# Kernel optimization log

Measured on AMD Instinct MI355X. Metric: run time of the kernel, lower is better.

The kernel has to match this reference:

```python
import jax, jax.numpy as jnp
import numpy as np

N_NODES = 100000
N_EDGES = 640000
D = 128
N_LAYERS = 4
N_GRAPHS = 512


def setup_inputs() -> dict:
    key = jax.random.key(0)
    ks = jax.random.split(key, 12)
    x = jax.random.normal(ks[0], (N_NODES, D), dtype=jnp.float32)
    edge_index = jax.random.randint(ks[1], (2, N_EDGES), 0, N_NODES, dtype=jnp.int64)
    batch = jnp.sort(jax.random.randint(ks[2], (N_NODES,), 0, N_GRAPHS, dtype=jnp.int64))
    s = 1.0 / np.sqrt(D)
    convW = jax.random.uniform(ks[3], (N_LAYERS, D, D), jnp.float32, -s, s)
    convB = jax.random.uniform(ks[4], (N_LAYERS, D), jnp.float32, -s, s)
    W1 = jax.random.uniform(ks[5], (D, D), jnp.float32, -s, s)
    b1 = jax.random.uniform(ks[6], (D,), jnp.float32, -s, s)
    W2 = jax.random.uniform(ks[7], (D, D), jnp.float32, -s, s)
    b2 = jax.random.uniform(ks[8], (D,), jnp.float32, -s, s)
    W3 = jax.random.uniform(ks[9], (D, 1), jnp.float32, -s, s)
    b3 = jax.random.uniform(ks[10], (1,), jnp.float32, -s, s)
    return {"x": x, "edge_index": edge_index, "batch": batch,
            "convW": convW, "convB": convB,
            "W1": W1, "b1": b1, "W2": W2, "b2": b2, "W3": W3, "b3": b3}


def reference(x, edge_index, batch, convW, convB, W1, b1, W2, b2, W3, b3):
    N = x.shape[0]
    # GCNConv default: add self-loops, symmetric deg^-1/2 normalization
    loops = jnp.arange(N, dtype=edge_index.dtype)
    src = jnp.concatenate([edge_index[0], loops])  # [E+N]
    dst = jnp.concatenate([edge_index[1], loops])
    deg = jax.ops.segment_sum(jnp.ones_like(dst, dtype=x.dtype), dst, num_segments=N)
    dinv = jnp.where(deg > 0, jax.lax.rsqrt(deg), 0.0)
    norm = (dinv[src] * dinv[dst])[:, None]  # [E+N, 1]
    h = x
    for i in range(N_LAYERS):
        hw = h @ convW[i]                                   # [N, D]
        msg = hw[src] * norm                                # gather + scale [E+N, D]
        agg = jax.ops.segment_sum(msg, dst, num_segments=N)  # scatter-add [N, D]
        h = jax.nn.relu(agg + convB[i])
    pooled = jax.ops.segment_sum(h, batch, num_segments=N_GRAPHS)  # [G, D]
    z = jax.nn.relu(pooled @ W1 + b1)
    z = jax.nn.relu(z @ W2 + b2)
    return jax.nn.sigmoid(z @ W3 + b3)  # [G, 1]
```

## Files before the change

### kernel.cpp

```cpp
#include <hip/hip_runtime.h>
#include <math.h>

#define D 128
#define LSTRIDE 136

typedef _Float16 half8 __attribute__((ext_vector_type(8)));
typedef _Float16 half4v __attribute__((ext_vector_type(4)));
typedef float f32x4 __attribute__((ext_vector_type(4)));


__global__ void k_fat1(const int* __restrict__ ei, int* __restrict__ counts,
                       int* __restrict__ pidx, int E, int countBlocks,
                       const float* __restrict__ convW, _Float16* __restrict__ Wf) {
    if ((int)blockIdx.x < countBlocks) {
        int e0 = (blockIdx.x * blockDim.x + threadIdx.x) * 4;
        if (e0 + 3 < E) {
            int4 d4 = *(const int4*)(ei + E + e0);
            int4 p;
            p.x = atomicAdd(&counts[d4.x], 1);
            p.y = atomicAdd(&counts[d4.y], 1);
            p.z = atomicAdd(&counts[d4.z], 1);
            p.w = atomicAdd(&counts[d4.w], 1);
            *(int4*)(pidx + e0) = p;
        } else {
            for (int e = e0; e < E; e++) pidx[e] = atomicAdd(&counts[ei[E + e]], 1);
        }
    } else {
        const int bid = blockIdx.x - countBlocks;
        const int l = bid >> 3;
        const int slot = (bid & 7) * 256 + threadIdx.x;
        const float* W = convW + (size_t)l * D * D;
        const int p = slot >> 6, ln = slot & 63;
        const int s = p >> 3, c = p & 7;
        const int kbase = s * 32 + ((ln >> 4) << 3);
        const int n = (c << 4) + (ln & 15);
        half8 hv;
#pragma unroll
        for (int j = 0; j < 8; j++) hv[j] = (_Float16)W[(size_t)(kbase + j) * D + n];
        *(half8*)(Wf + (size_t)l * D * D + (size_t)slot * 8) = hv;
    }
}

__global__ __launch_bounds__(256) void k_scan1(const int* __restrict__ counts,
                                               int* __restrict__ rowptrP,
                                               int* __restrict__ bsums,
                                               float* __restrict__ dinv,
                                               int* __restrict__ degHist, int N) {
    __shared__ int sh[256];
    __shared__ int lh[64];
    const int t = threadIdx.x;
    const int base = blockIdx.x * 1024 + t * 4;
    int c[4], pj[4];
#pragma unroll
    for (int j = 0; j < 4; j++) {
        c[j] = (base + j < N) ? counts[base + j] : 0;
        pj[j] = (c[j] + 3) & ~3;
    }
#pragma unroll
    for (int j = 0; j < 4; j++)
        if (base + j < N) dinv[base + j] = rsqrtf((float)(c[j] + 1));

    if (t < 64) lh[t] = 0;
    __syncthreads();
#pragma unroll
    for (int j = 0; j < 4; j++)
        if (base + j < N) atomicAdd(&lh[c[j] < 63 ? c[j] : 63], 1);
    __syncthreads();
    if (t < 64 && lh[t]) atomicAdd(&degHist[t], lh[t]);

    int tsum = pj[0] + pj[1] + pj[2] + pj[3];
    sh[t] = tsum;
    __syncthreads();
    for (int off = 1; off < 256; off <<= 1) {
        int v = (t >= off) ? sh[t - off] : 0;
        __syncthreads();
        sh[t] += v;
        __syncthreads();
    }
    int run = (t == 0) ? 0 : sh[t - 1];
    if (t == 255) bsums[blockIdx.x] = sh[255];
#pragma unroll
    for (int j = 0; j < 4; j++) {
        if (base + j <= N) rowptrP[base + j] = run;
        run += pj[j];
    }
}


__global__ __launch_bounds__(256) void k_fat2(int* __restrict__ rowptrP,
                                              const int* __restrict__ counts,
                                              const int* __restrict__ bsums,
                                              int NB, int N, int scanBlocks, int NS,
                                              int* __restrict__ srcs,
                                              const int* __restrict__ degHist,
                                              int* __restrict__ degCur,
                                              int* __restrict__ perm,
                                              int* __restrict__ rankOf) {
    if ((int)blockIdx.x < scanBlocks) {
        __shared__ int pre[128];
        const int t = threadIdx.x;
        if (t < 128) pre[t] = (t < NB) ? bsums[t] : 0;
        __syncthreads();
        for (int off = 1; off < 128; off <<= 1) {
            int v = (t >= off && t < 128) ? pre[t - off] : 0;
            __syncthreads();
            if (t < 128) pre[t] += v;
            __syncthreads();
        }
        int i = blockIdx.x * blockDim.x + t;
        if (i <= N) {
            int b = i >> 10;
            int add = (b == 0) ? 0 : pre[b - 1];
            int rp = rowptrP[i] + add;
            rowptrP[i] = rp;
            if (i < N) {
                int c = counts[i];
                int re_ = rp + c;
                int pad = (-c) & 3;
                for (int k2 = 0; k2 < pad; k2++) srcs[re_ + k2] = NS;
            }
        }
    } else {
        __shared__ int lbase[64], lh[64], gb[64];
        const int t = threadIdx.x;
        const int i = ((int)blockIdx.x - scanBlocks) * blockDim.x + t;
        if (t < 64) lh[t] = 0;
        __syncthreads();
        int deg = 0, lrank = 0;
        const bool v = i < N;
        if (v) {
            int c = counts[i];
            deg = c < 63 ? c : 63;
            lrank = atomicAdd(&lh[deg], 1);
        }
        __syncthreads();
        if (t < 64) gb[t] = lh[t] ? atomicAdd(&degCur[t], lh[t]) : 0;
        if (t == 0) {
            int run = 0;
            for (int d = 63; d >= 0; d--) { lbase[d] = run; run += degHist[d]; }
        }
        __syncthreads();
        if (v) {
            int r = lbase[deg] + gb[deg] + lrank;
            perm[r] = i;
            rankOf[i] = r;
        }
    }
}


__global__ void k_fill(const int* __restrict__ ei, const int* __restrict__ rowptrP,
                       const int* __restrict__ pidx, int* __restrict__ srcs, int E,
                       int fillBlocks, int slotBlocks, int N, int NS,
                       const int* __restrict__ rankOf,
                       const int* __restrict__ perm,
                       const float* __restrict__ dinv,
                       int* __restrict__ rbegR, int* __restrict__ rpenR,
                       float* __restrict__ dinvR, int* __restrict__ sentIdx,
                       const float* __restrict__ x,
                       _Float16* __restrict__ gA, _Float16* __restrict__ gB) {
    const int b = blockIdx.x;
    if (b < fillBlocks) {
        int e0 = (b * blockDim.x + threadIdx.x) * 4;
        if (e0 + 3 < E) {
            int4 s4 = *(const int4*)(ei + e0);
            int4 d4 = *(const int4*)(ei + E + e0);
            int4 p4 = *(const int4*)(pidx + e0);
            srcs[rowptrP[d4.x] + p4.x] = rankOf[s4.x];
            srcs[rowptrP[d4.y] + p4.y] = rankOf[s4.y];
            srcs[rowptrP[d4.z] + p4.z] = rankOf[s4.z];
            srcs[rowptrP[d4.w] + p4.w] = rankOf[s4.w];
        } else {
            for (int e = e0; e < E; e++)
                srcs[rowptrP[ei[E + e]] + pidx[e]] = rankOf[ei[e]];
        }
    } else if (b < fillBlocks + slotBlocks) {
        const int r = (b - fillBlocks) * blockDim.x + threadIdx.x;
        if (r == 0) { int4 sv; sv.x = sv.y = sv.z = sv.w = NS; *(int4*)sentIdx = sv; }
        if (r < NS) {
            if (r < N) {
                int p = perm[r];
                rbegR[r] = rowptrP[p];
                rpenR[r] = rowptrP[p + 1];
                dinvR[r] = dinv[p];
            } else {
                rbegR[r] = 0; rpenR[r] = 0; dinvR[r] = 0.f;
            }
        }
    } else {
        const int i = (b - fillBlocks - slotBlocks) * blockDim.x + threadIdx.x;
        const int TC = (NS + 1) * 16;
        if (i >= TC) return;
        const int row = i >> 4, j = i & 15;
        if (row < N) {
            const float s = dinv[row];
            const int rr = rankOf[row];
            const float4 v0 = *(const float4*)(x + (size_t)row * D + j * 8);
            const float4 v1 = *(const float4*)(x + (size_t)row * D + j * 8 + 4);
            half8 h;
            h[0] = (_Float16)(v0.x * s); h[1] = (_Float16)(v0.y * s);
            h[2] = (_Float16)(v0.z * s); h[3] = (_Float16)(v0.w * s);
            h[4] = (_Float16)(v1.x * s); h[5] = (_Float16)(v1.y * s);
            h[6] = (_Float16)(v1.z * s); h[7] = (_Float16)(v1.w * s);
            *(half8*)(gA + (size_t)rr * D + j * 8) = h;
        } else {
            half8 z;
#pragma unroll
            for (int j2 = 0; j2 < 8; j2++) z[j2] = (_Float16)0.f;
            *(half8*)(gA + (size_t)row * D + j * 8) = z;
            *(half8*)(gB + (size_t)row * D + j * 8) = z;
        }
    }
}


__global__ __launch_bounds__(256) void k_layer(
        const _Float16* __restrict__ gin,
        const int* __restrict__ rbegR, const int* __restrict__ rpenR,
        const int* __restrict__ srcs,
        const int* __restrict__ sentIdx,
        const float* __restrict__ dinvR,
        const int* __restrict__ perm,
        const _Float16* __restrict__ Wf,
        const float* __restrict__ bias,
        _Float16* __restrict__ gout, int N, int last) {
    __shared__ _Float16 S[64 * LSTRIDE];
    __shared__ _Float16 WL[D * D];

    const int tid  = threadIdx.x;
    const int w    = tid >> 6;
    const int lane = tid & 63;
    const int q    = lane >> 4;
    const int l16  = lane & 15;
    const int sb   = blockIdx.x * 64;
    const int cb   = l16 * 8;
    const int slot0 = sb + w * 16 + q * 4;

#pragma unroll 2
    for (int i = 0; i < 8; i++) {
        const int slot = i * 256 + tid;
        half8 wv = *(const half8*)(Wf + (size_t)slot * 8);
        *(half8*)(&WL[(size_t)slot * 8]) = wv;
    }

    int bg[4], nc[4];
    int mx = 0;
#pragma unroll
    for (int it = 0; it < 4; it++) {
        bg[it] = rbegR[slot0 + it];
        nc[it] = (rpenR[slot0 + it] - bg[it]) >> 2;
        mx = nc[it] > mx ? nc[it] : mx;
    }

    float a[4][8];
#pragma unroll
    for (int it = 0; it < 4; it++) {
        half8 sv = *(const half8*)(gin + (size_t)(slot0 + it) * D + cb);
#pragma unroll
        for (int j = 0; j < 8; j++) a[it][j] = (float)sv[j];
    }

    int4 cur[4];
#pragma unroll
    for (int it = 0; it < 4; it++) {
        const int* ip = (0 < nc[it]) ? (srcs + bg[it]) : sentIdx;
        cur[it] = *(const int4*)ip;
    }
    for (int ch = 0; ch < mx; ch++) {
        int4 nxt[4];
#pragma unroll
        for (int it = 0; it < 4; it++) {
            const int* ip = (ch + 1 < nc[it]) ? (srcs + bg[it] + (ch + 1) * 4) : sentIdx;
            nxt[it] = *(const int4*)ip;
        }
#pragma unroll
        for (int it = 0; it < 4; it++) {
            half8 v0 = *(const half8*)(gin + (size_t)cur[it].x * D + cb);
            half8 v1 = *(const half8*)(gin + (size_t)cur[it].y * D + cb);
            half8 v2 = *(const half8*)(gin + (size_t)cur[it].z * D + cb);
            half8 v3 = *(const half8*)(gin + (size_t)cur[it].w * D + cb);
#pragma unroll
            for (int j = 0; j < 8; j++)
                a[it][j] += ((float)v0[j] + (float)v1[j]) + ((float)v2[j] + (float)v3[j]);
        }
#pragma unroll
        for (int it = 0; it < 4; it++) cur[it] = nxt[it];
    }

#pragma unroll
    for (int it = 0; it < 4; it++) {
        const float sc = dinvR[slot0 + it];
        const int nl = w * 16 + q * 4 + it;
        half8 o;
#pragma unroll
        for (int j = 0; j < 8; j++) o[j] = (_Float16)(a[it][j] * sc);
        *(half8*)(&S[nl * LSTRIDE + cb]) = o;
    }

    __syncthreads();

    f32x4 acc[8];
#pragma unroll
    for (int cc = 0; cc < 8; cc++) acc[cc] = (f32x4){0.f, 0.f, 0.f, 0.f};

    const int nl2 = w * 16 + l16;
#pragma unroll
    for (int s = 0; s < 4; s++) {
        half8 bf = *(const half8*)(&S[nl2 * LSTRIDE + s * 32 + q * 8]);
#pragma unroll
        for (int cc = 0; cc < 8; cc++) {
            half8 wh = *(const half8*)(&WL[(size_t)((s * 8 + cc) * 64 + lane) * 8]);
            acc[cc] = __builtin_amdgcn_mfma_f32_16x16x32_f16(wh, bf, acc[cc], 0, 0, 0);
        }
    }

    const int slot2 = sb + nl2;
    if (!last) {
        const float scale = dinvR[slot2];
        _Float16* rp = gout + (size_t)slot2 * D + q * 4;
#pragma unroll
        for (int cc = 0; cc < 8; cc++) {
            const float4 bc = *(const float4*)(bias + cc * 16 + q * 4);
            half4v o;
            o[0] = (_Float16)(fmaxf(acc[cc][0] + bc.x, 0.f) * scale);
            o[1] = (_Float16)(fmaxf(acc[cc][1] + bc.y, 0.f) * scale);
            o[2] = (_Float16)(fmaxf(acc[cc][2] + bc.z, 0.f) * scale);
            o[3] = (_Float16)(fmaxf(acc[cc][3] + bc.w, 0.f) * scale);
            *(half4v*)(rp + cc * 16) = o;
        }
    } else if (slot2 < N) {
        const int node2 = perm[slot2];
        _Float16* rp = gout + (size_t)node2 * D + q * 4;
#pragma unroll
        for (int cc = 0; cc < 8; cc++) {
            const float4 bc = *(const float4*)(bias + cc * 16 + q * 4);
            half4v o;
            o[0] = (_Float16)fmaxf(acc[cc][0] + bc.x, 0.f);
            o[1] = (_Float16)fmaxf(acc[cc][1] + bc.y, 0.f);
            o[2] = (_Float16)fmaxf(acc[cc][2] + bc.z, 0.f);
            o[3] = (_Float16)fmaxf(acc[cc][3] + bc.w, 0.f);
            *(half4v*)(rp + cc * 16) = o;
        }
    }
}


__global__ __launch_bounds__(256) void k_poolhead(
        const _Float16* __restrict__ h, const int* __restrict__ batch,
        const float* __restrict__ W1, const float* __restrict__ b1,
        const float* __restrict__ W2, const float* __restrict__ b2,
        const float* __restrict__ W3, const float* __restrict__ b3,
        float* __restrict__ out, int N) {
    __shared__ int sb[2];
    __shared__ float part[16][D];
    __shared__ float pool[D];
    __shared__ float z[D];
    __shared__ float red[D];
    __shared__ float pr[2][D];

    const int g = blockIdx.x;
    const int t = threadIdx.x;

    if (t < 2) {
        int target = g + t;
        int lo = 0, hi = N;
        while (lo < hi) {
            int mid = (lo + hi) >> 1;
            if (batch[mid] < target) lo = mid + 1; else hi = mid;
        }
        sb[t] = lo;
    }
    __syncthreads();
    const int rs = sb[0], re = sb[1];

    const int w = t >> 6;
    const int lane = t & 63;
    const int rw = w * 4 + (lane >> 4);
    const int c8 = (lane & 15) * 8;

    float ax[8];
#pragma unroll
    for (int j = 0; j < 8; j++) ax[j] = 0.f;
    for (int r = rs + rw; r < re; r += 16) {
        half8 vv = *(const half8*)(h + (size_t)r * D + c8);
#pragma unroll
        for (int j = 0; j < 8; j++) ax[j] += (float)vv[j];
    }
#pragma unroll
    for (int j = 0; j < 8; j++) part[rw][c8 + j] = ax[j];
    __syncthreads();

    if (t < D) {
        float s = 0.f;
#pragma unroll
        for (int gg = 0; gg < 16; gg++) s += part[gg][t];
        pool[t] = s;
    }
    __syncthreads();

    {
        const int hf = t >> 7, tt = t & 127;
        const int k0 = hf * 64;
        float s = 0.f;
        for (int k = k0; k < k0 + 64; k++) s = fmaf(pool[k], W1[(size_t)k * D + tt], s);
        pr[hf][tt] = s;
    }
    __syncthreads();
    if (t < D) z[t] = fmaxf(pr[0][t] + pr[1][t] + b1[t], 0.f);
    __syncthreads();

    {
        const int hf = t >> 7, tt = t & 127;
        const int k0 = hf * 64;
        float s = 0.f;
        for (int k = k0; k < k0 + 64; k++) s = fmaf(z[k], W2[(size_t)k * D + tt], s);
        pr[hf][tt] = s;
    }
    __syncthreads();
    if (t < D) red[t] = fmaxf(pr[0][t] + pr[1][t] + b2[t], 0.f) * W3[t];
    __syncthreads();
    for (int off = 64; off >= 1; off >>= 1) {
        if (t < off) red[t] += red[t + off];
        __syncthreads();
    }
    if (t == 0) out[g] = 1.f / (1.f + expf(-(red[0] + b3[0])));
}


extern "C" void kernel_launch(void* const* d_in, const int* in_sizes, int n_in,
                              void* d_out, int out_size, void* d_ws, size_t ws_size,
                              hipStream_t stream) {
    const float* x     = (const float*)d_in[0];
    const int*   ei    = (const int*)d_in[1];
    const int*   batch = (const int*)d_in[2];
    const float* convW = (const float*)d_in[3];
    const float* convB = (const float*)d_in[4];
    const float* W1 = (const float*)d_in[5];
    const float* b1 = (const float*)d_in[6];
    const float* W2 = (const float*)d_in[7];
    const float* b2 = (const float*)d_in[8];
    const float* W3 = (const float*)d_in[9];
    const float* b3 = (const float*)d_in[10];
    float* out = (float*)d_out;

    const int N = in_sizes[0] / D;
    const int E = in_sizes[1] / 2;
    const int G = out_size;
    const int NB = (N + 1023) / 1024;
    const int NS = ((N + 63) / 64) * 64;

    char* w = (char*)d_ws;
    size_t off = 0;
    auto alloc = [&](size_t bytes) -> char* {
        char* p = w + off;
        off += (bytes + 255) & ~(size_t)255;
        return p;
    };
    float*     dinv   = (float*)alloc((size_t)N * 4);
    _Float16*  gA     = (_Float16*)alloc((size_t)(NS + 1) * D * 2);
    _Float16*  gB     = (_Float16*)alloc((size_t)(NS + 1) * D * 2);
    _Float16*  Wf     = (_Float16*)alloc((size_t)4 * D * D * 2);
    int*       counts = (int*)alloc((size_t)(N + 128) * 4);
    int*       degHist= counts + N;
    int*       degCur = counts + N + 64;
    int*       rowptrP= (int*)alloc((size_t)(N + 1) * 4);
    int*       pidx   = (int*)alloc((size_t)E * 4);
    int*       srcs   = (int*)alloc((size_t)(E + 3 * N) * 4);
    int*       bsums  = (int*)alloc((size_t)NB * 4);
    int*       perm   = (int*)alloc((size_t)N * 4);
    int*       rankOf = (int*)alloc((size_t)N * 4);
    int*       rbegR  = (int*)alloc((size_t)NS * 4);
    int*       rpenR  = (int*)alloc((size_t)NS * 4);
    float*     dinvR  = (float*)alloc((size_t)NS * 4);
    int*       sentIdx= (int*)alloc(16);

    hipMemsetAsync(counts, 0, (size_t)(N + 128) * 4, stream);
    const int countBlocks = (E / 4 + 255) / 256;
    k_fat1<<<countBlocks + 32, 256, 0, stream>>>(ei, counts, pidx, E, countBlocks,
                                                 convW, Wf);
    k_scan1<<<NB, 256, 0, stream>>>(counts, rowptrP, bsums, dinv, degHist, N);
    const int scanBlocks = (N + 1 + 255) / 256;
    const int rankBlocks = (N + 255) / 256;
    k_fat2<<<scanBlocks + rankBlocks, 256, 0, stream>>>(rowptrP, counts, bsums, NB, N,
                                                        scanBlocks, NS, srcs,
                                                        degHist, degCur, perm, rankOf);
    const int fillBlocks = (E / 4 + 255) / 256;
    const int slotBlocks = (NS + 255) / 256;
    const int cvtBlocks  = ((NS + 1) * 16 + 255) / 256;
    k_fill<<<fillBlocks + slotBlocks + cvtBlocks, 256, 0, stream>>>(
        ei, rowptrP, pidx, srcs, E, fillBlocks, slotBlocks, N, NS,
        rankOf, perm, dinv, rbegR, rpenR, dinvR, sentIdx, x, gA, gB);

    const int layer_grid = NS / 64;
    const _Float16* gi = gA;
    _Float16* go = gB;
    for (int l = 0; l < 4; l++) {
        k_layer<<<layer_grid, 256, 0, stream>>>(gi, rbegR, rpenR, srcs, sentIdx,
                                                dinvR, perm,
                                                Wf + (size_t)l * D * D,
                                                convB + (size_t)l * D,
                                                go, N, l == 3);
        const _Float16* tmp = go;
        go = (_Float16*)gi;
        gi = tmp;
    }

    k_poolhead<<<G, 256, 0, stream>>>(gi, batch, W1, b1, W2, b2, W3, b3, out, N);
}
```

Before: 358.7 us.

## Halve layer tile size, read weights from global, merge fill row work

```diff
diff --git a/kernel.cpp b/kernel.cpp
--- a/kernel.cpp
+++ b/kernel.cpp
@@ -151,7 +151,7 @@
 
 __global__ void k_fill(const int* __restrict__ ei, const int* __restrict__ rowptrP,
                        const int* __restrict__ pidx, int* __restrict__ srcs, int E,
-                       int fillBlocks, int slotBlocks, int N, int NS,
+                       int fillBlocks, int N, int NS,
                        const int* __restrict__ rankOf,
                        const int* __restrict__ perm,
                        const float* __restrict__ dinv,
@@ -174,29 +174,37 @@
             for (int e = e0; e < E; e++)
                 srcs[rowptrP[ei[E + e]] + pidx[e]] = rankOf[ei[e]];
         }
-    } else if (b < fillBlocks + slotBlocks) {
-        const int r = (b - fillBlocks) * blockDim.x + threadIdx.x;
-        if (r == 0) { int4 sv; sv.x = sv.y = sv.z = sv.w = NS; *(int4*)sentIdx = sv; }
-        if (r < NS) {
+    } else {
+        __shared__ int pS[16];
+        __shared__ float dS[16];
+        const int base = (b - fillBlocks) * 16;
+        const int t = threadIdx.x;
+        if (t == 0 && base == 0) {
+            int4 sv; sv.x = sv.y = sv.z = sv.w = NS; *(int4*)sentIdx = sv;
+        }
+        if (t < 16) {
+            const int r = base + t;
+            int p = -1; float dv = 0.f;
             if (r < N) {
-                int p = perm[r];
+                p = perm[r];
                 rbegR[r] = rowptrP[p];
                 rpenR[r] = rowptrP[p + 1];
-                dinvR[r] = dinv[p];
-            } else {
+                dv = dinv[p];
+                dinvR[r] = dv;
+            } else if (r < NS) {
                 rbegR[r] = 0; rpenR[r] = 0; dinvR[r] = 0.f;
             }
-        }
-    } else {
-        const int i = (b - fillBlocks - slotBlocks) * blockDim.x + threadIdx.x;
-        const int TC = (NS + 1) * 16;
-        if (i >= TC) return;
-        const int row = i >> 4, j = i & 15;
-        if (row < N) {
-            const float s = dinv[row];
-            const int rr = rankOf[row];
-            const float4 v0 = *(const float4*)(x + (size_t)row * D + j * 8);
-            const float4 v1 = *(const float4*)(x + (size_t)row * D + j * 8 + 4);
+            pS[t] = p; dS[t] = dv;
+        }
+        __syncthreads();
+        const int rr = base + (t >> 4);
+        if (rr > NS) return;
+        const int j = t & 15;
+        const int p = pS[t >> 4];
+        if (p >= 0) {
+            const float s = dS[t >> 4];
+            const float4 v0 = *(const float4*)(x + (size_t)p * D + j * 8);
+            const float4 v1 = *(const float4*)(x + (size_t)p * D + j * 8 + 4);
             half8 h;
             h[0] = (_Float16)(v0.x * s); h[1] = (_Float16)(v0.y * s);
             h[2] = (_Float16)(v0.z * s); h[3] = (_Float16)(v0.w * s);
@@ -207,14 +215,14 @@
             half8 z;
 #pragma unroll
             for (int j2 = 0; j2 < 8; j2++) z[j2] = (_Float16)0.f;
-            *(half8*)(gA + (size_t)row * D + j * 8) = z;
-            *(half8*)(gB + (size_t)row * D + j * 8) = z;
-        }
-    }
-}
-
-
-__global__ __launch_bounds__(256) void k_layer(
+            *(half8*)(gA + (size_t)rr * D + j * 8) = z;
+            *(half8*)(gB + (size_t)rr * D + j * 8) = z;
+        }
+    }
+}
+
+
+__global__ __launch_bounds__(256, 8) void k_layer(
         const _Float16* __restrict__ gin,
         const int* __restrict__ rbegR, const int* __restrict__ rpenR,
         const int* __restrict__ srcs,
@@ -224,57 +232,49 @@
         const _Float16* __restrict__ Wf,
         const float* __restrict__ bias,
         _Float16* __restrict__ gout, int N, int last) {
-    __shared__ _Float16 S[64 * LSTRIDE];
-    __shared__ _Float16 WL[D * D];
+    __shared__ _Float16 S[32 * LSTRIDE];
 
     const int tid  = threadIdx.x;
     const int w    = tid >> 6;
     const int lane = tid & 63;
     const int q    = lane >> 4;
     const int l16  = lane & 15;
-    const int sb   = blockIdx.x * 64;
+    const int sb   = blockIdx.x * 32;
     const int cb   = l16 * 8;
-    const int slot0 = sb + w * 16 + q * 4;
-
-#pragma unroll 2
-    for (int i = 0; i < 8; i++) {
-        const int slot = i * 256 + tid;
-        half8 wv = *(const half8*)(Wf + (size_t)slot * 8);
-        *(half8*)(&WL[(size_t)slot * 8]) = wv;
-    }
-
-    int bg[4], nc[4];
+    const int slot0 = sb + w * 8 + q * 2;
+
+    int bg[2], nc[2];
     int mx = 0;
 #pragma unroll
-    for (int it = 0; it < 4; it++) {
+    for (int it = 0; it < 2; it++) {
         bg[it] = rbegR[slot0 + it];
         nc[it] = (rpenR[slot0 + it] - bg[it]) >> 2;
         mx = nc[it] > mx ? nc[it] : mx;
     }
 
-    float a[4][8];
-#pragma unroll
-    for (int it = 0; it < 4; it++) {
+    float a[2][8];
+#pragma unroll
+    for (int it = 0; it < 2; it++) {
         half8 sv = *(const half8*)(gin + (size_t)(slot0 + it) * D + cb);
 #pragma unroll
         for (int j = 0; j < 8; j++) a[it][j] = (float)sv[j];
     }
 
-    int4 cur[4];
-#pragma unroll
-    for (int it = 0; it < 4; it++) {
+    int4 cur[2];
+#pragma unroll
+    for (int it = 0; it < 2; it++) {
         const int* ip = (0 < nc[it]) ? (srcs + bg[it]) : sentIdx;
         cur[it] = *(const int4*)ip;
     }
     for (int ch = 0; ch < mx; ch++) {
-        int4 nxt[4];
-#pragma unroll
-        for (int it = 0; it < 4; it++) {
+        int4 nxt[2];
+#pragma unroll
+        for (int it = 0; it < 2; it++) {
             const int* ip = (ch + 1 < nc[it]) ? (srcs + bg[it] + (ch + 1) * 4) : sentIdx;
             nxt[it] = *(const int4*)ip;
         }
 #pragma unroll
-        for (int it = 0; it < 4; it++) {
+        for (int it = 0; it < 2; it++) {
             half8 v0 = *(const half8*)(gin + (size_t)cur[it].x * D + cb);
             half8 v1 = *(const half8*)(gin + (size_t)cur[it].y * D + cb);
             half8 v2 = *(const half8*)(gin + (size_t)cur[it].z * D + cb);
@@ -284,13 +284,13 @@
                 a[it][j] += ((float)v0[j] + (float)v1[j]) + ((float)v2[j] + (float)v3[j]);
         }
 #pragma unroll
-        for (int it = 0; it < 4; it++) cur[it] = nxt[it];
-    }
-
-#pragma unroll
-    for (int it = 0; it < 4; it++) {
+        for (int it = 0; it < 2; it++) cur[it] = nxt[it];
+    }
+
+#pragma unroll
+    for (int it = 0; it < 2; it++) {
         const float sc = dinvR[slot0 + it];
-        const int nl = w * 16 + q * 4 + it;
+        const int nl = w * 8 + q * 2 + it;
         half8 o;
 #pragma unroll
         for (int j = 0; j < 8; j++) o[j] = (_Float16)(a[it][j] * sc);
@@ -299,18 +299,20 @@
 
     __syncthreads();
 
-    f32x4 acc[8];
-#pragma unroll
-    for (int cc = 0; cc < 8; cc++) acc[cc] = (f32x4){0.f, 0.f, 0.f, 0.f};
-
-    const int nl2 = w * 16 + l16;
+    f32x4 acc[4];
+#pragma unroll
+    for (int c2 = 0; c2 < 4; c2++) acc[c2] = (f32x4){0.f, 0.f, 0.f, 0.f};
+
+    const int tile = w >> 1;
+    const int ccb  = (w & 1) * 4;
+    const int nl2  = tile * 16 + l16;
 #pragma unroll
     for (int s = 0; s < 4; s++) {
         half8 bf = *(const half8*)(&S[nl2 * LSTRIDE + s * 32 + q * 8]);
 #pragma unroll
-        for (int cc = 0; cc < 8; cc++) {
-            half8 wh = *(const half8*)(&WL[(size_t)((s * 8 + cc) * 64 + lane) * 8]);
-            acc[cc] = __builtin_amdgcn_mfma_f32_16x16x32_f16(wh, bf, acc[cc], 0, 0, 0);
+        for (int c2 = 0; c2 < 4; c2++) {
+            half8 wh = *(const half8*)(Wf + (size_t)((s * 8 + ccb + c2) * 64 + lane) * 8);
+            acc[c2] = __builtin_amdgcn_mfma_f32_16x16x32_f16(wh, bf, acc[c2], 0, 0, 0);
         }
     }
 
@@ -319,26 +321,28 @@
         const float scale = dinvR[slot2];
         _Float16* rp = gout + (size_t)slot2 * D + q * 4;
 #pragma unroll
-        for (int cc = 0; cc < 8; cc++) {
+        for (int c2 = 0; c2 < 4; c2++) {
+            const int cc = ccb + c2;
             const float4 bc = *(const float4*)(bias + cc * 16 + q * 4);
             half4v o;
-            o[0] = (_Float16)(fmaxf(acc[cc][0] + bc.x, 0.f) * scale);
-            o[1] = (_Float16)(fmaxf(acc[cc][1] + bc.y, 0.f) * scale);
-            o[2] = (_Float16)(fmaxf(acc[cc][2] + bc.z, 0.f) * scale);
-            o[3] = (_Float16)(fmaxf(acc[cc][3] + bc.w, 0.f) * scale);
+            o[0] = (_Float16)(fmaxf(acc[c2][0] + bc.x, 0.f) * scale);
+            o[1] = (_Float16)(fmaxf(acc[c2][1] + bc.y, 0.f) * scale);
+            o[2] = (_Float16)(fmaxf(acc[c2][2] + bc.z, 0.f) * scale);
+            o[3] = (_Float16)(fmaxf(acc[c2][3] + bc.w, 0.f) * scale);
             *(half4v*)(rp + cc * 16) = o;
         }
     } else if (slot2 < N) {
         const int node2 = perm[slot2];
         _Float16* rp = gout + (size_t)node2 * D + q * 4;
 #pragma unroll
-        for (int cc = 0; cc < 8; cc++) {
+        for (int c2 = 0; c2 < 4; c2++) {
+            const int cc = ccb + c2;
             const float4 bc = *(const float4*)(bias + cc * 16 + q * 4);
             half4v o;
-            o[0] = (_Float16)fmaxf(acc[cc][0] + bc.x, 0.f);
-            o[1] = (_Float16)fmaxf(acc[cc][1] + bc.y, 0.f);
-            o[2] = (_Float16)fmaxf(acc[cc][2] + bc.z, 0.f);
-            o[3] = (_Float16)fmaxf(acc[cc][3] + bc.w, 0.f);
+            o[0] = (_Float16)fmaxf(acc[c2][0] + bc.x, 0.f);
+            o[1] = (_Float16)fmaxf(acc[c2][1] + bc.y, 0.f);
+            o[2] = (_Float16)fmaxf(acc[c2][2] + bc.z, 0.f);
+            o[3] = (_Float16)fmaxf(acc[c2][3] + bc.w, 0.f);
             *(half4v*)(rp + cc * 16) = o;
         }
     }
@@ -485,13 +489,12 @@
                                                         scanBlocks, NS, srcs,
                                                         degHist, degCur, perm, rankOf);
     const int fillBlocks = (E / 4 + 255) / 256;
-    const int slotBlocks = (NS + 255) / 256;
-    const int cvtBlocks  = ((NS + 1) * 16 + 255) / 256;
-    k_fill<<<fillBlocks + slotBlocks + cvtBlocks, 256, 0, stream>>>(
-        ei, rowptrP, pidx, srcs, E, fillBlocks, slotBlocks, N, NS,
+    const int rowBlocks  = (NS + 16) / 16;
+    k_fill<<<fillBlocks + rowBlocks, 256, 0, stream>>>(
+        ei, rowptrP, pidx, srcs, E, fillBlocks, N, NS,
         rankOf, perm, dinv, rbegR, rpenR, dinvR, sentIdx, x, gA, gB);
 
-    const int layer_grid = NS / 64;
+    const int layer_grid = NS / 32;
     const _Float16* gi = gA;
     _Float16* go = gB;
     for (int l = 0; l < 4; l++) {
```

After: 344.6 us. -3.9%, faster.
